# Optimization experiments

Measured on AMD Instinct MI355X. Metric: run time of the kernel, lower is better.

The kernel has to match this reference:

```python
import jax, jax.numpy as jnp
import numpy as np

PI_2 = 3.14159 / 2  # matches the torch module's pi_2 constant
EPS = 1e-8          # F.cosine_similarity default eps


def setup_inputs() -> dict:
    key = jax.random.key(0)
    k1, k2 = jax.random.split(key)
    B, N, C, H, W = 32, 2000, 512, 7, 7
    key_t = jax.random.normal(k1, (B, C, H, W), dtype=jnp.float32)
    memory = jax.random.normal(k2, (N, C, H, W), dtype=jnp.float32)
    return {"key": key_t, "memory": memory}


def reference(key, memory):
    # Memory.read(key): cosine-similarity addressing + tan warp + softmax, then weighted read.
    B = key.shape[0]
    N = memory.shape[0]
    k = key.reshape(B, -1)        # [B, D], D = C*H*W
    m = memory.reshape(N, -1)     # [N, D]
    # cosine similarity with torch's eps clamping on norms
    dots = jnp.einsum('bd,nd->bn', k, m)                                   # [B, N]
    k_norm = jnp.maximum(jnp.sqrt(jnp.sum(k * k, axis=-1, keepdims=True)), EPS)  # [B, 1]
    m_norm = jnp.maximum(jnp.sqrt(jnp.sum(m * m, axis=-1)), EPS)                 # [N]
    cos = dots / (k_norm * m_norm[None, :])                                 # [B, N]
    w = jax.nn.softmax(jnp.tan(cos * PI_2), axis=1)                         # [B, N]
    # weighted read: sum_n w[b,n] * memory[n,c,h,w] -> [B, C, H, W]
    out = jnp.einsum('bn,nchw->bchw', w, memory)
    return out
```

## Files before the change

### kernel.cpp

```cpp
#include <hip/hip_runtime.h>
#include <math.h>

#define D_ELEMS 25088
#define D4      6272
#define N_MEM   2000
#define B_KEYS  32
#define PI_2F   1.570795f
#define EPSF    1e-8f


__global__ __launch_bounds__(256) void k_dots(const float* __restrict__ key,
                                              const float* __restrict__ mem,
                                              float* __restrict__ dots_part,
                                              float* __restrict__ mn2_part) {
    const int nb   = blockIdx.x / 7;
    const int s    = blockIdx.x % 7;
    const int n0   = nb * 8;
    const int bg   = threadIdx.x >> 6;
    const int lane = threadIdx.x & 63;

    const float4* K4 = (const float4*)key;
    const float4* M4 = (const float4*)mem;

    float acc[8][8];
#pragma unroll
    for (int j = 0; j < 8; ++j)
#pragma unroll
        for (int i = 0; i < 8; ++i) acc[j][i] = 0.f;
    float msq[8] = {0.f,0.f,0.f,0.f,0.f,0.f,0.f,0.f};

    const int c0 = s * 14;
    for (int c = 0; c < 14; ++c) {
        const int d4 = (c0 + c) * 64 + lane;
        float4 kf[8], mf[8];
#pragma unroll
        for (int i = 0; i < 8; ++i) kf[i] = K4[(bg * 8 + i) * D4 + d4];
#pragma unroll
        for (int j = 0; j < 8; ++j) mf[j] = M4[(n0 + j) * D4 + d4];
#pragma unroll
        for (int j = 0; j < 8; ++j) {
#pragma unroll
            for (int i = 0; i < 8; ++i) {
                acc[j][i] += mf[j].x * kf[i].x + mf[j].y * kf[i].y
                           + mf[j].z * kf[i].z + mf[j].w * kf[i].w;
            }
        }
        if (bg == 0) {
#pragma unroll
            for (int j = 0; j < 8; ++j)
                msq[j] += mf[j].x * mf[j].x + mf[j].y * mf[j].y
                        + mf[j].z * mf[j].z + mf[j].w * mf[j].w;
        }
    }

#pragma unroll
    for (int off = 8; off < 64; off <<= 1)
#pragma unroll
        for (int j = 0; j < 8; ++j)
#pragma unroll
            for (int i = 0; i < 8; ++i)
                acc[j][i] += __shfl_xor(acc[j][i], off, 64);

    __shared__ float red[4][8][65];
    if (lane < 8) {
#pragma unroll
        for (int j = 0; j < 8; ++j)
#pragma unroll
            for (int i = 0; i < 8; ++i)
                red[bg][lane][j * 8 + i] = acc[j][i];
    }
    __syncthreads();

    float ssum = red[bg][0][lane];
#pragma unroll
    for (int i = 1; i < 8; ++i) ssum += red[bg][i][lane];
    dots_part[(size_t)(s * N_MEM + n0 + (lane >> 3)) * B_KEYS + bg * 8 + (lane & 7)] = ssum;

    if (bg == 0) {
#pragma unroll
        for (int off = 1; off < 64; off <<= 1)
#pragma unroll
            for (int j = 0; j < 8; ++j)
                msq[j] += __shfl_xor(msq[j], off, 64);
        if (lane == 0) {
#pragma unroll
            for (int j = 0; j < 8; ++j) mn2_part[s * N_MEM + n0 + j] = msq[j];
        }
    }
}

__global__ __launch_bounds__(512) void k_softmax(const float* __restrict__ key,
                                                 const float* __restrict__ dots_part,
                                                 const float* __restrict__ mn2_part,
                                                 float* __restrict__ w) {
    const int b   = blockIdx.x;
    const int tid = threadIdx.x;
    __shared__ float sred[512];
    __shared__ float xbuf[N_MEM];

    const float4* K4 = (const float4*)(key + (size_t)b * D_ELEMS);
    float ks = 0.f;
    for (int i = tid; i < D4; i += 512) {
        float4 kf = K4[i];
        ks += kf.x * kf.x + kf.y * kf.y + kf.z * kf.z + kf.w * kf.w;
    }
    sred[tid] = ks;
    __syncthreads();
    for (int o = 256; o; o >>= 1) {
        if (tid < o) sred[tid] += sred[tid + o];
        __syncthreads();
    }
    const float knorm = fmaxf(sqrtf(sred[0]), EPSF);
    __syncthreads();

    float mx = -1e30f;
    for (int n = tid; n < N_MEM; n += 512) {
        float ds = 0.f, ms = 0.f;
#pragma unroll
        for (int s = 0; s < 7; ++s) ds += dots_part[(size_t)(s * N_MEM + n) * B_KEYS + b];
#pragma unroll
        for (int s = 0; s < 7; ++s) ms += mn2_part[s * N_MEM + n];
        float mn = fmaxf(sqrtf(ms), EPSF);
        float x  = __tanf((ds / (knorm * mn)) * PI_2F);
        xbuf[n] = x;
        mx = fmaxf(mx, x);
    }
    sred[tid] = mx;
    __syncthreads();
    for (int o = 256; o; o >>= 1) {
        if (tid < o) sred[tid] = fmaxf(sred[tid], sred[tid + o]);
        __syncthreads();
    }
    mx = sred[0];
    __syncthreads();

    float sm = 0.f;
    for (int n = tid; n < N_MEM; n += 512) sm += __expf(xbuf[n] - mx);
    sred[tid] = sm;
    __syncthreads();
    for (int o = 256; o; o >>= 1) {
        if (tid < o) sred[tid] += sred[tid + o];
        __syncthreads();
    }
    const float inv = 1.f / sred[0];
    __syncthreads();

    for (int n = tid; n < N_MEM; n += 512)
        w[n * B_KEYS + b] = __expf(xbuf[n] - mx) * inv;
}

__global__ __launch_bounds__(256) void k_read(const float* __restrict__ mem,
                                              const float* __restrict__ w,
                                              float* __restrict__ partial,
                                              int nPerS) {
    const int db   = blockIdx.x % 98;
    const int s    = blockIdx.x / 98;
    const int n0   = s * nPerS;
    const int bg   = threadIdx.x >> 6;
    const int lane = threadIdx.x & 63;
    const int d4   = db * 64 + lane;

    const float4* M4 = (const float4*)mem;
    const float4* W4 = (const float4*)w;
    __shared__ float4 wls4[250 * 8];

    float acc[8][4];
#pragma unroll
    for (int i = 0; i < 8; ++i)
#pragma unroll
        for (int j = 0; j < 4; ++j) acc[i][j] = 0.f;

    for (int c0 = 0; c0 < nPerS; c0 += 250) {
        const int cn = min(250, nPerS - c0);
        __syncthreads();
        for (int i = threadIdx.x; i < cn * 8; i += 256)
            wls4[i] = W4[(n0 + c0) * 8 + i];
        __syncthreads();

        float4 mv = M4[(size_t)(n0 + c0) * D4 + d4];
        float4 wa = wls4[bg * 2];
        float4 wb = wls4[bg * 2 + 1];
        for (int nn = 0; nn < cn; ++nn) {
            const float4 mc = mv, wac = wa, wbc = wb;
            const int nx = (nn + 1 < cn) ? nn + 1 : nn;
            mv = M4[(size_t)(n0 + c0 + nx) * D4 + d4];
            wa = wls4[nx * 8 + bg * 2];
            wb = wls4[nx * 8 + bg * 2 + 1];
            const float wv[8] = {wac.x, wac.y, wac.z, wac.w,
                                 wbc.x, wbc.y, wbc.z, wbc.w};
#pragma unroll
            for (int i = 0; i < 8; ++i) {
                acc[i][0] += wv[i] * mc.x;
                acc[i][1] += wv[i] * mc.y;
                acc[i][2] += wv[i] * mc.z;
                acc[i][3] += wv[i] * mc.w;
            }
        }
    }

    float4* P4 = (float4*)partial;
#pragma unroll
    for (int i = 0; i < 8; ++i)
        P4[(size_t)(s * B_KEYS + bg * 8 + i) * D4 + d4] =
            make_float4(acc[i][0], acc[i][1], acc[i][2], acc[i][3]);
}

__global__ __launch_bounds__(256) void k_finish(const float* __restrict__ partial,
                                                float* __restrict__ out, int ns) {
    const int i = blockIdx.x * 256 + threadIdx.x;
    const float4* P4 = (const float4*)partial;
    float4 sum = P4[i];
    for (int s = 1; s < ns; ++s) {
        const float4 p = P4[(size_t)s * (B_KEYS * D4) + i];
        sum.x += p.x; sum.y += p.y; sum.z += p.z; sum.w += p.w;
    }
    ((float4*)out)[i] = sum;
}

extern "C" void kernel_launch(void* const* d_in, const int* in_sizes, int n_in,
                              void* d_out, int out_size, void* d_ws, size_t ws_size,
                              hipStream_t stream) {
    (void)in_sizes; (void)n_in; (void)out_size;
    const float* key = (const float*)d_in[0];
    const float* mem = (const float*)d_in[1];
    float* out = (float*)d_out;
    float* ws  = (float*)d_ws;

    float* dots_part = ws;
    float* mn2_part  = ws + 448000;
    float* w         = ws + 462016;
    float* part      = ws + 526080;

    int ns = 8;
    while (ns > 1 && (size_t)(526080 + (size_t)ns * 802816) * 4 > ws_size) ns >>= 1;
    const int nPerS = N_MEM / ns;

    k_dots   <<<1750, 256, 0, stream>>>(key, mem, dots_part, mn2_part);
    k_softmax<<<B_KEYS, 512, 0, stream>>>(key, dots_part, mn2_part, w);
    k_read   <<<98 * ns, 256, 0, stream>>>(mem, w, part, nPerS);
    k_finish <<<784, 256, 0, stream>>>(part, out, ns);
}
```

Baseline: 439.2 us.

## Compute key-memory dot products with bf16 MFMA instead of fp32 FMA

Result: faster. 420.3 us (-4.3%).

```diff
diff --git a/kernel.cpp b/kernel.cpp
--- a/kernel.cpp
+++ b/kernel.cpp
@@ -7,86 +7,81 @@
 #define B_KEYS  32
 #define PI_2F   1.570795f
 #define EPSF    1e-8f
-
-
-__global__ __launch_bounds__(256) void k_dots(const float* __restrict__ key,
-                                              const float* __restrict__ mem,
-                                              float* __restrict__ dots_part,
-                                              float* __restrict__ mn2_part) {
-    const int nb   = blockIdx.x / 7;
-    const int s    = blockIdx.x % 7;
-    const int n0   = nb * 8;
-    const int bg   = threadIdx.x >> 6;
-    const int lane = threadIdx.x & 63;
-
-    const float4* K4 = (const float4*)key;
-    const float4* M4 = (const float4*)mem;
-
-    float acc[8][8];
-#pragma unroll
-    for (int j = 0; j < 8; ++j)
-#pragma unroll
-        for (int i = 0; i < 8; ++i) acc[j][i] = 0.f;
-    float msq[8] = {0.f,0.f,0.f,0.f,0.f,0.f,0.f,0.f};
-
-    const int c0 = s * 14;
-    for (int c = 0; c < 14; ++c) {
-        const int d4 = (c0 + c) * 64 + lane;
-        float4 kf[8], mf[8];
-#pragma unroll
-        for (int i = 0; i < 8; ++i) kf[i] = K4[(bg * 8 + i) * D4 + d4];
-#pragma unroll
-        for (int j = 0; j < 8; ++j) mf[j] = M4[(n0 + j) * D4 + d4];
-#pragma unroll
-        for (int j = 0; j < 8; ++j) {
-#pragma unroll
-            for (int i = 0; i < 8; ++i) {
-                acc[j][i] += mf[j].x * kf[i].x + mf[j].y * kf[i].y
-                           + mf[j].z * kf[i].z + mf[j].w * kf[i].w;
-            }
+#define NSLICE  8
+#define KSLICE  3136
+#define KSTEPS  98
+
+using short8 = __attribute__((ext_vector_type(8))) short;
+using short4v = __attribute__((ext_vector_type(4))) short;
+using f32x4  = __attribute__((ext_vector_type(4))) float;
+
+
+__device__ inline short f2bf(float x) {
+    union { float f; unsigned u; } v; v.f = x;
+    unsigned r = v.u + 0x7fffu + ((v.u >> 16) & 1u);
+    return (short)(r >> 16);
+}
+
+__global__ __launch_bounds__(256) void k_prep(const float* __restrict__ key,
+                                              short* __restrict__ keyb) {
+    const int i = blockIdx.x * 256 + threadIdx.x;
+    const float4 f = ((const float4*)key)[i];
+    short4v s; s[0] = f2bf(f.x); s[1] = f2bf(f.y); s[2] = f2bf(f.z); s[3] = f2bf(f.w);
+    ((short4v*)keyb)[i] = s;
+}
+
+__global__ __launch_bounds__(64) void k_dots_mfma(const short* __restrict__ keyb,
+                                                  const float* __restrict__ mem,
+                                                  float* __restrict__ dots_part,
+                                                  float* __restrict__ mn2_part) {
+    const int nt   = blockIdx.x / NSLICE;
+    const int s    = blockIdx.x % NSLICE;
+    const int n0   = nt * 16;
+    const int lane = threadIdx.x;
+    const int quad = lane >> 4;
+    const int l16  = lane & 15;
+    const int k0   = s * KSLICE + quad * 8;
+
+    const short* a0p = keyb + (size_t)l16 * D_ELEMS + k0;
+    const short* a1p = keyb + (size_t)(16 + l16) * D_ELEMS + k0;
+    const float4* bp = (const float4*)(mem + (size_t)(n0 + l16) * D_ELEMS + k0);
+
+    f32x4 acc0 = {0.f, 0.f, 0.f, 0.f};
+    f32x4 acc1 = {0.f, 0.f, 0.f, 0.f};
+    float msq = 0.f;
+
+    short8 a0 = *(const short8*)a0p;
+    short8 a1 = *(const short8*)a1p;
+    float4 f0 = bp[0], f1 = bp[1];
+
+    for (int t = 0; t < KSTEPS; ++t) {
+        const short8 a0c = a0, a1c = a1;
+        const float4 f0c = f0, f1c = f1;
+        if (t + 1 < KSTEPS) {
+            const int ko = (t + 1) * 8;
+            a0 = *(const short8*)(a0p + (t + 1) * 32);
+            a1 = *(const short8*)(a1p + (t + 1) * 32);
+            f0 = bp[ko]; f1 = bp[ko + 1];
         }
-        if (bg == 0) {
-#pragma unroll
-            for (int j = 0; j < 8; ++j)
-                msq[j] += mf[j].x * mf[j].x + mf[j].y * mf[j].y
-                        + mf[j].z * mf[j].z + mf[j].w * mf[j].w;
-        }
-    }
-
-#pragma unroll
-    for (int off = 8; off < 64; off <<= 1)
-#pragma unroll
-        for (int j = 0; j < 8; ++j)
-#pragma unroll
-            for (int i = 0; i < 8; ++i)
-                acc[j][i] += __shfl_xor(acc[j][i], off, 64);
-
-    __shared__ float red[4][8][65];
-    if (lane < 8) {
-#pragma unroll
-        for (int j = 0; j < 8; ++j)
-#pragma unroll
-            for (int i = 0; i < 8; ++i)
-                red[bg][lane][j * 8 + i] = acc[j][i];
-    }
-    __syncthreads();
-
-    float ssum = red[bg][0][lane];
-#pragma unroll
-    for (int i = 1; i < 8; ++i) ssum += red[bg][i][lane];
-    dots_part[(size_t)(s * N_MEM + n0 + (lane >> 3)) * B_KEYS + bg * 8 + (lane & 7)] = ssum;
-
-    if (bg == 0) {
-#pragma unroll
-        for (int off = 1; off < 64; off <<= 1)
-#pragma unroll
-            for (int j = 0; j < 8; ++j)
-                msq[j] += __shfl_xor(msq[j], off, 64);
-        if (lane == 0) {
-#pragma unroll
-            for (int j = 0; j < 8; ++j) mn2_part[s * N_MEM + n0 + j] = msq[j];
-        }
-    }
+        msq += f0c.x * f0c.x + f0c.y * f0c.y + f0c.z * f0c.z + f0c.w * f0c.w
+             + f1c.x * f1c.x + f1c.y * f1c.y + f1c.z * f1c.z + f1c.w * f1c.w;
+        short8 b;
+        b[0] = f2bf(f0c.x); b[1] = f2bf(f0c.y); b[2] = f2bf(f0c.z); b[3] = f2bf(f0c.w);
+        b[4] = f2bf(f1c.x); b[5] = f2bf(f1c.y); b[6] = f2bf(f1c.z); b[7] = f2bf(f1c.w);
+        acc0 = __builtin_amdgcn_mfma_f32_16x16x32_bf16(a0c, b, acc0, 0, 0, 0);
+        acc1 = __builtin_amdgcn_mfma_f32_16x16x32_bf16(a1c, b, acc1, 0, 0, 0);
+    }
+
+    float* dp = dots_part + (size_t)(s * N_MEM + n0 + l16) * B_KEYS;
+#pragma unroll
+    for (int r = 0; r < 4; ++r) {
+        dp[quad * 4 + r]      = acc0[r];
+        dp[16 + quad * 4 + r] = acc1[r];
+    }
+
+    msq += __shfl_xor(msq, 16, 64);
+    msq += __shfl_xor(msq, 32, 64);
+    if (lane < 16) mn2_part[s * N_MEM + n0 + lane] = msq;
 }
 
 __global__ __launch_bounds__(512) void k_softmax(const float* __restrict__ key,
@@ -117,9 +112,9 @@
     for (int n = tid; n < N_MEM; n += 512) {
         float ds = 0.f, ms = 0.f;
 #pragma unroll
-        for (int s = 0; s < 7; ++s) ds += dots_part[(size_t)(s * N_MEM + n) * B_KEYS + b];
-#pragma unroll
-        for (int s = 0; s < 7; ++s) ms += mn2_part[s * N_MEM + n];
+        for (int s = 0; s < NSLICE; ++s) ds += dots_part[(size_t)(s * N_MEM + n) * B_KEYS + b];
+#pragma unroll
+        for (int s = 0; s < NSLICE; ++s) ms += mn2_part[s * N_MEM + n];
         float mn = fmaxf(sqrtf(ms), EPSF);
         float x  = __tanf((ds / (knorm * mn)) * PI_2F);
         xbuf[n] = x;
@@ -226,17 +221,19 @@
     float* out = (float*)d_out;
     float* ws  = (float*)d_ws;
 
-    float* dots_part = ws;
-    float* mn2_part  = ws + 448000;
-    float* w         = ws + 462016;
-    float* part      = ws + 526080;
+    short* keyb      = (short*)ws;
+    float* dots_part = ws + 401408;
+    float* mn2_part  = ws + 913408;
+    float* w         = ws + 929408;
+    float* part      = ws + 993408;
 
     int ns = 8;
-    while (ns > 1 && (size_t)(526080 + (size_t)ns * 802816) * 4 > ws_size) ns >>= 1;
+    while (ns > 1 && (size_t)(993408 + (size_t)ns * 802816) * 4 > ws_size) ns >>= 1;
     const int nPerS = N_MEM / ns;
 
-    k_dots   <<<1750, 256, 0, stream>>>(key, mem, dots_part, mn2_part);
-    k_softmax<<<B_KEYS, 512, 0, stream>>>(key, dots_part, mn2_part, w);
-    k_read   <<<98 * ns, 256, 0, stream>>>(mem, w, part, nPerS);
-    k_finish <<<784, 256, 0, stream>>>(part, out, ns);
-}
+    k_prep     <<<784, 256, 0, stream>>>(key, keyb);
+    k_dots_mfma<<<125 * NSLICE, 64, 0, stream>>>(keyb, mem, dots_part, mn2_part);
+    k_softmax  <<<B_KEYS, 512, 0, stream>>>(key, dots_part, mn2_part, w);
+    k_read     <<<98 * ns, 256, 0, stream>>>(mem, w, part, nPerS);
+    k_finish   <<<784, 256, 0, stream>>>(part, out, ns);
+}
```
